# Kernel tuning notes

Hardware: AMD Instinct MI355X
Metric: run time of the kernel (lower is better)

Reference implementation:

```python
import jax, jax.numpy as jnp
import numpy as np

OUT = (7, 7, 7)      # output_size (D_out, H_out, W_out)
SCALE = 1.0          # spatial_scale


def setup_inputs() -> dict:
    key = jax.random.key(0)
    k1, k2 = jax.random.split(key)
    B, C, D, H, W = 2, 256, 64, 64, 64
    N = 512
    features = jax.random.normal(k1, (B, C, D, H, W), dtype=jnp.float32)
    p = jax.random.uniform(k2, (B, N, 6), dtype=jnp.float32) * 63.0
    lo = jnp.minimum(p[..., :3], p[..., 3:])
    hi = jnp.maximum(p[..., :3], p[..., 3:])
    proposals = jnp.concatenate([lo, hi], axis=-1)  # (B, N, 6) valid boxes
    return {"features": features, "proposals": proposals}


def _trilinear(vol, gz, gy, gx):
    # vol: (C, D, H, W); gz/gy/gx: (Do, Ho, Wo) voxel-space coords.
    # grid_sample(mode='bilinear', padding_mode='zeros', align_corners=True)
    C, D, H, W = vol.shape
    z0f, y0f, x0f = jnp.floor(gz), jnp.floor(gy), jnp.floor(gx)
    wz, wy, wx = gz - z0f, gy - y0f, gx - x0f
    z0, y0, x0 = z0f.astype(jnp.int32), y0f.astype(jnp.int32), x0f.astype(jnp.int32)

    def gather(zi, yi, xi):
        valid = (zi >= 0) & (zi < D) & (yi >= 0) & (yi < H) & (xi >= 0) & (xi < W)
        v = vol[:, jnp.clip(zi, 0, D - 1), jnp.clip(yi, 0, H - 1), jnp.clip(xi, 0, W - 1)]
        return v * valid.astype(vol.dtype)[None]  # (C, Do, Ho, Wo)

    out = jnp.zeros((C,) + gz.shape, dtype=vol.dtype)
    for dz in (0, 1):
        for dy in (0, 1):
            for dx in (0, 1):
                w = ((wz if dz else 1.0 - wz)
                     * (wy if dy else 1.0 - wy)
                     * (wx if dx else 1.0 - wx))
                out = out + gather(z0 + dz, y0 + dy, x0 + dx) * w[None]
    return out


def reference(features, proposals):
    # features: (B, C, D, H, W); proposals: (B, N, 6) [x1,y1,z1,x2,y2,z2]
    B, C, D, H, W = features.shape
    Do, Ho, Wo = OUT

    def one_roi(vol, prop):
        p = prop * SCALE
        x1, y1, z1, x2, y2, z2 = p[0], p[1], p[2], p[3], p[4], p[5]
        zc = jnp.linspace(z1, z2, Do)
        yc = jnp.linspace(y1, y2, Ho)
        xc = jnp.linspace(x1, x2, Wo)
        gz, gy, gx = jnp.meshgrid(zc, yc, xc, indexing='ij')  # (Do,Ho,Wo)
        return _trilinear(vol, gz, gy, gx)  # (C, Do, Ho, Wo)

    per_batch = jax.vmap(lambda vol, props: jax.vmap(lambda p: one_roi(vol, p))(props))
    out = per_batch(features, proposals)  # (B, N, C, Do, Ho, Wo)
    return out.reshape(B * proposals.shape[1], C, Do, Ho, Wo)
```

## Files before the change

### kernel.cpp

```cpp
#include <hip/hip_runtime.h>
#include <hip/hip_fp16.h>


#define B_      2
#define C_      256
#define N_      512
#define NENT    (N_ * 7)
#define SP      66
#define PLANE_S (64 * SP)
#define CHUNK   3
#define NCHUNK  21
#define THREADS 1024
#define GROUPS  20
#define REC_F_BASE 128
#define WS_NEEDED ((size_t)REC_F_BASE * 4 + (size_t)B_ * NENT * 8 * 4)

typedef _Float16 h2v __attribute__((ext_vector_type(2)));

__device__ __forceinline__ float gcoord(float lo, float hi, int i) {
    return lo + (hi - lo) * (1.0f / 6.0f) * (float)i;
}

__device__ __forceinline__ uint32_t pkrtz(float a, float b) {
    auto h = __builtin_amdgcn_cvt_pkrtz(a, b);
    return __builtin_bit_cast(uint32_t, h);
}

__device__ __forceinline__ float xlerp(uint32_t pkv, uint32_t pkw) {
#if __has_builtin(__builtin_amdgcn_fdot2)
    return __builtin_amdgcn_fdot2(__builtin_bit_cast(h2v, pkv),
                                  __builtin_bit_cast(h2v, pkw), 0.0f, false);
#else
    h2v v = __builtin_bit_cast(h2v, pkv);
    h2v w = __builtin_bit_cast(h2v, pkw);
    return (float)v[0] * (float)w[0] + (float)v[1] * (float)w[1];
#endif
}

__global__ __launch_bounds__(256) void bucket_kernel(
    const float* __restrict__ props, int* __restrict__ wsi, float* __restrict__ wsf)
{
    int b = blockIdx.x;
    __shared__ int counts[63];
    __shared__ int starts[64];
    __shared__ int cursors[63];
    int tid = threadIdx.x;
    if (tid < 63) counts[tid] = 0;
    __syncthreads();
    for (int e = tid; e < NENT; e += 256) {
        int n = e / 7, iz = e - n * 7;
        const float* pr = props + (size_t)(b * N_ + n) * 6;
        float gz = gcoord(pr[2], pr[5], iz);
        int z0 = min(max((int)gz, 0), 62);
        atomicAdd(&counts[z0], 1);
    }
    __syncthreads();
    if (tid == 0) {
        int s = 0;
        for (int k = 0; k < 63; ++k) { starts[k] = s; s += counts[k]; }
        starts[63] = s;
    }
    __syncthreads();
    if (tid < 63) cursors[tid] = starts[tid];
    __syncthreads();
    for (int e = tid; e < NENT; e += 256) {
        int n = e / 7, iz = e - n * 7;
        const float* pr = props + (size_t)(b * N_ + n) * 6;
        float x1p = pr[0], y1p = pr[1], z1p = pr[2];
        float x2p = pr[3], y2p = pr[4], z2p = pr[5];
        float gz = gcoord(z1p, z2p, iz);
        int z0 = min(max((int)gz, 0), 62);
        float wz = gz - (float)z0;
        int pos = atomicAdd(&cursors[z0], 1);
        int off = (b * N_ + n) * (C_ * 343) + iz * 49;
        float* r = wsf + REC_F_BASE + (size_t)(b * NENT + pos) * 8;
        r[0] = x1p; r[1] = (x2p - x1p) * (1.0f / 6.0f);
        r[2] = y1p; r[3] = (y2p - y1p) * (1.0f / 6.0f);
        r[4] = wz;  r[5] = __int_as_float(off);
        r[6] = __int_as_float(z0); r[7] = 0.0f;
    }
    if (tid < 64) wsi[b * 64 + tid] = starts[tid];
}

__global__ __launch_bounds__(THREADS, 8) void roialign3d_chunk_kernel(
    const float* __restrict__ feat,
    const int* __restrict__ wsi,
    const float* __restrict__ wsf,
    float* __restrict__ out)
{
    __shared__ __align__(16) uint32_t pk[4 * PLANE_S];

    int bid = blockIdx.x;
    int s = bid & 511;
    int k = bid >> 9;
    int b = s >> 8;
    int c = s & 255;
    int zlo = k * CHUNK;
    const float* vol = feat + (size_t)s * 262144 + (size_t)zlo * 4096;
    int tid = threadIdx.x;

    int base = wsi[b * 64 + zlo];
    int end  = wsi[b * 64 + zlo + CHUNK];

    float4 v0 = *(const float4*)(vol + 0 * 4096 + (tid << 2));
    float4 v1 = *(const float4*)(vol + 1 * 4096 + (tid << 2));
    float4 v2 = *(const float4*)(vol + 2 * 4096 + (tid << 2));
    float4 v3 = *(const float4*)(vol + 3 * 4096 + (tid << 2));

    int g = tid / 49;
    int p = tid - g * 49;
    int iy = p / 7;
    float fx = (float)(p - iy * 7);
    float fy = (float)iy;
    const float4* recs = (const float4*)(wsf + REC_F_BASE);
    const int rbase = b * NENT;
    int myEnd = (g < GROUPS) ? end : base;
    int e = base + g;
    float4 rA, rB, rAn, rBn;
    if (e < myEnd) {
        rA = recs[(size_t)(rbase + e) * 2];
        rB = recs[(size_t)(rbase + e) * 2 + 1];
        if (e + GROUPS < myEnd) {
            rAn = recs[(size_t)(rbase + e + GROUPS) * 2];
            rBn = recs[(size_t)(rbase + e + GROUPS) * 2 + 1];
        }
    }

    int swb = (tid >> 4) * SP + ((tid & 15) << 2);
#define STAGE_WRITE(slotBase, v, v4) do {                                   \
        uint2 w0 = make_uint2(pkrtz((v).x, (v).y), pkrtz((v).y, (v).z));    \
        uint2 w1 = make_uint2(pkrtz((v).z, (v).w), pkrtz((v).w, (v4)));     \
        *(uint2*)&pk[(slotBase) + swb]     = w0;                            \
        *(uint2*)&pk[(slotBase) + swb + 2] = w1;                            \
    } while (0)
    {
        float a0 = __shfl_down(v0.x, 1);
        float a1 = __shfl_down(v1.x, 1);
        float a2 = __shfl_down(v2.x, 1);
        float a3 = __shfl_down(v3.x, 1);
        STAGE_WRITE(0 * PLANE_S, v0, a0);
        STAGE_WRITE(1 * PLANE_S, v1, a1);
        STAGE_WRITE(2 * PLANE_S, v2, a2);
        STAGE_WRITE(3 * PLANE_S, v3, a3);
    }
#undef STAGE_WRITE
    __syncthreads();

    float* outc = out + (size_t)c * 343;
    while (e < myEnd) {
        float gx = fmaf(rA.y, fx, rA.x);
        float gy = fmaf(rA.w, fy, rA.z);
        int x0 = (int)gx, y0 = (int)gy;
        float wx = __builtin_amdgcn_fractf(gx);
        float wy = __builtin_amdgcn_fractf(gy);
        uint32_t pw = pkrtz(1.0f - wx, wx);
        float wz = rB.x;
        int offc = __float_as_int(rB.y);
        int lz = __float_as_int(rB.z) - zlo;
        int sl = lz * PLANE_S + y0 * SP + x0;
        uint32_t q0 = pk[sl],           q1 = pk[sl + SP];
        uint32_t q2 = pk[sl + PLANE_S], q3 = pk[sl + PLANE_S + SP];

        float4 tA = rAn, tB = rBn;
        int e2 = e + 2 * GROUPS;
        if (e2 < myEnd) {
            rAn = recs[(size_t)(rbase + e2) * 2];
            rBn = recs[(size_t)(rbase + e2) * 2 + 1];
        }

        float c00 = xlerp(q0, pw);
        float c01 = xlerp(q1, pw);
        float c10 = xlerp(q2, pw);
        float c11 = xlerp(q3, pw);
        float d0 = fmaf(c01 - c00, wy, c00);
        float d1 = fmaf(c11 - c10, wy, c10);
        outc[offc + p] = fmaf(d1 - d0, wz, d0);

        e += GROUPS; rA = tA; rB = tB;
    }
}

__global__ __launch_bounds__(128) void roialign3d_fallback(
    const float* __restrict__ feat, const float* __restrict__ props,
    float* __restrict__ out)
{
    int bid = blockIdx.x;
    int xcd = bid & 7;
    int j   = bid >> 3;
    int s   = xcd + ((j >> 9) << 3);
    int n   = j & 511;
    int b   = s >> 8;
    int c   = s & 255;
    const float* prop = props + ((size_t)(b * N_ + n)) * 6;
    float x1p = prop[0], y1p = prop[1], z1p = prop[2];
    float x2p = prop[3], y2p = prop[4], z2p = prop[5];
    float sx = (x2p - x1p) * (1.0f / 6.0f);
    float sy = (y2p - y1p) * (1.0f / 6.0f);
    float sz = (z2p - z1p) * (1.0f / 6.0f);
    const float* vol = feat + (size_t)s * (64 * 64 * 64);
    float* o = out + ((size_t)(b * N_ + n) * C_ + c) * 343;
    for (int p = threadIdx.x; p < 343; p += 128) {
        int iz = p / 49, r = p - iz * 49, iy = r / 7, ix = r - iy * 7;
        float gx = x1p + sx * ix, gy = y1p + sy * iy, gz = z1p + sz * iz;
        int x0 = (int)gx, y0 = (int)gy, z0 = (int)gz;
        float wx = gx - x0, wy = gy - y0, wz = gz - z0;
        int x1 = min(x0 + 1, 63), y1 = min(y0 + 1, 63), z1 = min(z0 + 1, 63);
        const float* p00 = vol + ((z0 * 64 + y0) << 6);
        const float* p01 = vol + ((z0 * 64 + y1) << 6);
        const float* p10 = vol + ((z1 * 64 + y0) << 6);
        const float* p11 = vol + ((z1 * 64 + y1) << 6);
        float c00 = p00[x0] + (p00[x1] - p00[x0]) * wx;
        float c01 = p01[x0] + (p01[x1] - p01[x0]) * wx;
        float c10 = p10[x0] + (p10[x1] - p10[x0]) * wx;
        float c11 = p11[x0] + (p11[x1] - p11[x0]) * wx;
        float d0 = c00 + (c01 - c00) * wy;
        float d1 = c10 + (c11 - c10) * wy;
        o[p] = d0 + (d1 - d0) * wz;
    }
}

extern "C" void kernel_launch(void* const* d_in, const int* in_sizes, int n_in,
                              void* d_out, int out_size, void* d_ws, size_t ws_size,
                              hipStream_t stream) {
    const float* feat  = (const float*)d_in[0];
    const float* props = (const float*)d_in[1];
    float* out = (float*)d_out;

    if (ws_size < WS_NEEDED) {
        roialign3d_fallback<<<B_ * C_ * N_, 128, 0, stream>>>(feat, props, out);
        return;
    }
    int*   wsi = (int*)d_ws;
    float* wsf = (float*)d_ws;
    bucket_kernel<<<B_, 256, 0, stream>>>(props, wsi, wsf);
    roialign3d_chunk_kernel<<<NCHUNK * 512, THREADS, 0, stream>>>(feat, wsi, wsf, out);
}
```

Baseline: 290.4 us.

## Process one z-slab for two channels per block with interleaved z-pair LDS

Each block now handles a single z0 slab (planes z0 and z0+1) for two adjacent channels, where before it handled a 3-slice chunk for one channel. Z0 and z0+1 values are interleaved into uint2 LDS entries so one 64-bit read fetches both z corners. Each record lookup and coordinate computation now yields two output channels, and blocks whose slab has no entries exit early. The cost is a grid of 63*256 blocks, each staging two planes per channel, so more total feature reads than the 3-slice chunking, which shared a boundary plane across slices.

```diff
diff --git a/kernel.cpp b/kernel.cpp
--- a/kernel.cpp
+++ b/kernel.cpp
@@ -7,9 +7,7 @@
 #define N_      512
 #define NENT    (N_ * 7)
 #define SP      66
-#define PLANE_S (64 * SP)
-#define CHUNK   3
-#define NCHUNK  21
+#define PLANE_P (64 * SP)
 #define THREADS 1024
 #define GROUPS  20
 #define REC_F_BASE 128
@@ -77,35 +75,37 @@
         r[0] = x1p; r[1] = (x2p - x1p) * (1.0f / 6.0f);
         r[2] = y1p; r[3] = (y2p - y1p) * (1.0f / 6.0f);
         r[4] = wz;  r[5] = __int_as_float(off);
-        r[6] = __int_as_float(z0); r[7] = 0.0f;
+        r[6] = 0.0f; r[7] = 0.0f;
     }
     if (tid < 64) wsi[b * 64 + tid] = starts[tid];
 }
 
-__global__ __launch_bounds__(THREADS, 8) void roialign3d_chunk_kernel(
+__global__ __launch_bounds__(THREADS, 8) void roialign3d_zpair_kernel(
     const float* __restrict__ feat,
     const int* __restrict__ wsi,
     const float* __restrict__ wsf,
     float* __restrict__ out)
 {
-    __shared__ __align__(16) uint32_t pk[4 * PLANE_S];
+    __shared__ __align__(16) uint2 pk2[2 * PLANE_P];
 
     int bid = blockIdx.x;
-    int s = bid & 511;
-    int k = bid >> 9;
-    int b = s >> 8;
-    int c = s & 255;
-    int zlo = k * CHUNK;
-    const float* vol = feat + (size_t)s * 262144 + (size_t)zlo * 4096;
+    int pi  = bid & 255;
+    int z0  = bid >> 8;
+    int b   = pi >> 7;
+    int c0  = (pi & 127) << 1;
     int tid = threadIdx.x;
 
-    int base = wsi[b * 64 + zlo];
-    int end  = wsi[b * 64 + zlo + CHUNK];
-
-    float4 v0 = *(const float4*)(vol + 0 * 4096 + (tid << 2));
-    float4 v1 = *(const float4*)(vol + 1 * 4096 + (tid << 2));
-    float4 v2 = *(const float4*)(vol + 2 * 4096 + (tid << 2));
-    float4 v3 = *(const float4*)(vol + 3 * 4096 + (tid << 2));
+    int base = wsi[b * 64 + z0];
+    int end  = wsi[b * 64 + z0 + 1];
+    if (base == end) return;
+
+    const float* vol0 = feat + ((size_t)((b << 8) + c0) << 18) + ((size_t)z0 << 12);
+    const float* vol1 = vol0 + (1 << 18);
+
+    float4 a0 = *(const float4*)(vol0 + (tid << 2));
+    float4 a1 = *(const float4*)(vol0 + 4096 + (tid << 2));
+    float4 b0 = *(const float4*)(vol1 + (tid << 2));
+    float4 b1 = *(const float4*)(vol1 + 4096 + (tid << 2));
 
     int g = tid / 49;
     int p = tid - g * 49;
@@ -126,27 +126,26 @@
         }
     }
 
-    int swb = (tid >> 4) * SP + ((tid & 15) << 2);
-#define STAGE_WRITE(slotBase, v, v4) do {                                   \
-        uint2 w0 = make_uint2(pkrtz((v).x, (v).y), pkrtz((v).y, (v).z));    \
-        uint2 w1 = make_uint2(pkrtz((v).z, (v).w), pkrtz((v).w, (v4)));     \
-        *(uint2*)&pk[(slotBase) + swb]     = w0;                            \
-        *(uint2*)&pk[(slotBase) + swb + 2] = w1;                            \
-    } while (0)
     {
-        float a0 = __shfl_down(v0.x, 1);
-        float a1 = __shfl_down(v1.x, 1);
-        float a2 = __shfl_down(v2.x, 1);
-        float a3 = __shfl_down(v3.x, 1);
-        STAGE_WRITE(0 * PLANE_S, v0, a0);
-        STAGE_WRITE(1 * PLANE_S, v1, a1);
-        STAGE_WRITE(2 * PLANE_S, v2, a2);
-        STAGE_WRITE(3 * PLANE_S, v3, a3);
-    }
-#undef STAGE_WRITE
-    __syncthreads();
-
-    float* outc = out + (size_t)c * 343;
+        int swb = (tid >> 4) * SP + ((tid & 15) << 2);
+        float a0n = __shfl_down(a0.x, 1);
+        float a1n = __shfl_down(a1.x, 1);
+        float b0n = __shfl_down(b0.x, 1);
+        float b1n = __shfl_down(b1.x, 1);
+        uint2* d0 = &pk2[swb];
+        uint2* d1 = &pk2[PLANE_P + swb];
+        d0[0] = make_uint2(pkrtz(a0.x, a0.y), pkrtz(a1.x, a1.y));
+        d0[1] = make_uint2(pkrtz(a0.y, a0.z), pkrtz(a1.y, a1.z));
+        d0[2] = make_uint2(pkrtz(a0.z, a0.w), pkrtz(a1.z, a1.w));
+        d0[3] = make_uint2(pkrtz(a0.w, a0n),  pkrtz(a1.w, a1n));
+        d1[0] = make_uint2(pkrtz(b0.x, b0.y), pkrtz(b1.x, b1.y));
+        d1[1] = make_uint2(pkrtz(b0.y, b0.z), pkrtz(b1.y, b1.z));
+        d1[2] = make_uint2(pkrtz(b0.z, b0.w), pkrtz(b1.z, b1.w));
+        d1[3] = make_uint2(pkrtz(b0.w, b0n),  pkrtz(b1.w, b1n));
+    }
+    __syncthreads();
+
+    float* outc = out + (size_t)c0 * 343;
     while (e < myEnd) {
         float gx = fmaf(rA.y, fx, rA.x);
         float gy = fmaf(rA.w, fy, rA.z);
@@ -156,10 +155,9 @@
         uint32_t pw = pkrtz(1.0f - wx, wx);
         float wz = rB.x;
         int offc = __float_as_int(rB.y);
-        int lz = __float_as_int(rB.z) - zlo;
-        int sl = lz * PLANE_S + y0 * SP + x0;
-        uint32_t q0 = pk[sl],           q1 = pk[sl + SP];
-        uint32_t q2 = pk[sl + PLANE_S], q3 = pk[sl + PLANE_S + SP];
+        int sl = y0 * SP + x0;
+        uint2 qa0 = pk2[sl],           qa1 = pk2[sl + SP];
+        uint2 qb0 = pk2[PLANE_P + sl], qb1 = pk2[PLANE_P + sl + SP];
 
         float4 tA = rAn, tB = rBn;
         int e2 = e + 2 * GROUPS;
@@ -168,13 +166,24 @@
             rBn = recs[(size_t)(rbase + e2) * 2 + 1];
         }
 
-        float c00 = xlerp(q0, pw);
-        float c01 = xlerp(q1, pw);
-        float c10 = xlerp(q2, pw);
-        float c11 = xlerp(q3, pw);
-        float d0 = fmaf(c01 - c00, wy, c00);
-        float d1 = fmaf(c11 - c10, wy, c10);
-        outc[offc + p] = fmaf(d1 - d0, wz, d0);
+        {
+            float c00 = xlerp(qa0.x, pw);
+            float c10 = xlerp(qa0.y, pw);
+            float c01 = xlerp(qa1.x, pw);
+            float c11 = xlerp(qa1.y, pw);
+            float d0 = fmaf(c01 - c00, wy, c00);
+            float d1 = fmaf(c11 - c10, wy, c10);
+            outc[offc + p] = fmaf(d1 - d0, wz, d0);
+        }
+        {
+            float c00 = xlerp(qb0.x, pw);
+            float c10 = xlerp(qb0.y, pw);
+            float c01 = xlerp(qb1.x, pw);
+            float c11 = xlerp(qb1.y, pw);
+            float d0 = fmaf(c01 - c00, wy, c00);
+            float d1 = fmaf(c11 - c10, wy, c10);
+            outc[offc + 343 + p] = fmaf(d1 - d0, wz, d0);
+        }
 
         e += GROUPS; rA = tA; rB = tB;
     }
@@ -233,5 +242,5 @@
     int*   wsi = (int*)d_ws;
     float* wsf = (float*)d_ws;
     bucket_kernel<<<B_, 256, 0, stream>>>(props, wsi, wsf);
-    roialign3d_chunk_kernel<<<NCHUNK * 512, THREADS, 0, stream>>>(feat, wsi, wsf, out);
-}
+    roialign3d_zpair_kernel<<<63 * 256, THREADS, 0, stream>>>(feat, wsi, wsf, out);
+}
```

After: 300.0 us, median of 2. 1.03x slower.
